# Optimization experiments

Hardware: AMD Instinct MI355X
Metric: run time of the kernel (lower is better)

Reference implementation:

```python
import jax, jax.numpy as jnp
import numpy as np

DIM = 768
HEADS = 12
HIDDEN = 3072
EPS = 1e-5


def _layernorm(x, g, b):
    mu = jnp.mean(x, axis=-1, keepdims=True)
    var = jnp.var(x, axis=-1, keepdims=True)
    return (x - mu) * jax.lax.rsqrt(var + EPS) * g + b


def setup_inputs() -> dict:
    key = jax.random.key(0)
    ks = jax.random.split(key, 10)
    s_in = 1.0 / np.sqrt(DIM)
    s_hid = 1.0 / np.sqrt(HIDDEN)
    return {
        "x": jax.random.normal(ks[0], (8, 1024, DIM), dtype=jnp.float32),
        "ln1_g": jnp.ones((DIM,), jnp.float32),
        "ln1_b": jnp.zeros((DIM,), jnp.float32),
        "qkv_w": jax.random.uniform(ks[1], (DIM, 3 * DIM), jnp.float32, -s_in, s_in),
        "qkv_b": jnp.zeros((3 * DIM,), jnp.float32),
        "proj_w": jax.random.uniform(ks[2], (DIM, DIM), jnp.float32, -s_in, s_in),
        "proj_b": jnp.zeros((DIM,), jnp.float32),
        "ln2_g": jnp.ones((DIM,), jnp.float32),
        "ln2_b": jnp.zeros((DIM,), jnp.float32),
        "fc1_w": jax.random.uniform(ks[3], (DIM, HIDDEN), jnp.float32, -s_in, s_in),
        "fc1_b": jnp.zeros((HIDDEN,), jnp.float32),
        "fc2_w": jax.random.uniform(ks[4], (HIDDEN, DIM), jnp.float32, -s_hid, s_hid),
        "fc2_b": jnp.zeros((DIM,), jnp.float32),
    }


def reference(x, ln1_g, ln1_b, qkv_w, qkv_b, proj_w, proj_b,
              ln2_g, ln2_b, fc1_w, fc1_b, fc2_w, fc2_b):
    B, N, C = x.shape
    H = HEADS
    Dh = C // H
    scale = Dh ** -0.5

    # --- attention sublayer (pre-norm) ---
    h = _layernorm(x, ln1_g, ln1_b)
    qkv = h @ qkv_w + qkv_b  # [B,N,3C]
    qkv = qkv.reshape(B, N, 3, H, Dh)
    q = qkv[:, :, 0].transpose(0, 2, 1, 3)  # [B,H,N,Dh]
    k = qkv[:, :, 1].transpose(0, 2, 1, 3)
    v = qkv[:, :, 2].transpose(0, 2, 1, 3)
    attn = jax.nn.softmax(jnp.einsum('bhnd,bhmd->bhnm', q, k) * scale, axis=-1)
    o = jnp.einsum('bhnm,bhmd->bhnd', attn, v)  # [B,H,N,Dh]
    o = o.transpose(0, 2, 1, 3).reshape(B, N, C)
    x = x + (o @ proj_w + proj_b)

    # --- MLP sublayer (pre-norm) ---
    h = _layernorm(x, ln2_g, ln2_b)
    h = jax.nn.gelu(h @ fc1_w + fc1_b, approximate=False)
    x = x + (h @ fc2_w + fc2_b)
    return x
```

## Files before the change

kernel.cpp:

```cpp
#include <hip/hip_runtime.h>
#include <math.h>

#define DIM    768
#define HEADS  12
#define HIDDEN 3072
#define SEQ    1024
#define NTOK   8192
#define QKVLD  2304

typedef __bf16 bf16_t;
typedef __bf16 bf16x4 __attribute__((ext_vector_type(4)));
typedef __bf16 bf16x8 __attribute__((ext_vector_type(8)));
typedef float  f32x4  __attribute__((ext_vector_type(4)));

union ABFrag { bf16x4 h[2]; bf16x8 v; };

__device__ __forceinline__ void gload16(const void* g, void* l) {
  __builtin_amdgcn_global_load_lds(
      (const __attribute__((address_space(1))) void*)g,
      (__attribute__((address_space(3))) void*)l, 16, 0, 0);
}

__device__ __forceinline__ f32x4 mfma16(bf16x8 a, bf16x8 b, f32x4 c) {
  return __builtin_amdgcn_mfma_f32_16x16x32_bf16(a, b, c, 0, 0, 0);
}

__device__ __forceinline__ ABFrag load_frag(const bf16_t* rowp, int g) {
  ABFrag f;
  f.h[0] = *(const bf16x4*)(rowp + 4 * g);
  f.h[1] = *(const bf16x4*)(rowp + 4 * g + 16);
  return f;
}

__device__ __forceinline__ ABFrag load_frag_swz(const bf16_t* base, int row, int e, int g) {
  const int o0 = e + 4 * g, o1 = o0 + 16;
  const int s = row & 7;
  const bf16_t* rp = base + row * 64;
  ABFrag f;
  f.h[0] = *(const bf16x4*)(rp + ((((o0 >> 3) ^ s) << 3) | (o0 & 7)));
  f.h[1] = *(const bf16x4*)(rp + ((((o1 >> 3) ^ s) << 3) | (o1 & 7)));
  return f;
}

__device__ __forceinline__ bf16x8 ldsfrag(const bf16_t* base, int row, int lc) {
  return *(const bf16x8*)(base + row * 64 + (((lc ^ (row & 7))) << 3));
}

__global__ __launch_bounds__(256) void ln_kernel(
    const float* __restrict__ x, const float* __restrict__ gw,
    const float* __restrict__ bw, bf16_t* __restrict__ out) {
  const int row = blockIdx.x;
  const int t = threadIdx.x;
  const float* xr = x + (size_t)row * DIM;
  float v0 = xr[t], v1 = xr[t + 256], v2 = xr[t + 512];
  float s = v0 + v1 + v2;
  float s2 = v0 * v0 + v1 * v1 + v2 * v2;
  #pragma unroll
  for (int o = 32; o > 0; o >>= 1) {
    s += __shfl_down(s, o);
    s2 += __shfl_down(s2, o);
  }
  __shared__ float red[8];
  if ((t & 63) == 0) { red[(t >> 6) * 2] = s; red[(t >> 6) * 2 + 1] = s2; }
  __syncthreads();
  float S  = red[0] + red[2] + red[4] + red[6];
  float S2 = red[1] + red[3] + red[5] + red[7];
  float mu  = S * (1.0f / DIM);
  float var = S2 * (1.0f / DIM) - mu * mu;
  float rs  = rsqrtf(var + 1e-5f);
  bf16_t* orow = out + (size_t)row * DIM;
  orow[t]       = (bf16_t)((v0 - mu) * rs * gw[t]       + bw[t]);
  orow[t + 256] = (bf16_t)((v1 - mu) * rs * gw[t + 256] + bw[t + 256]);
  orow[t + 512] = (bf16_t)((v2 - mu) * rs * gw[t + 512] + bw[t + 512]);
}

__global__ __launch_bounds__(256) void wtrans_kernel(
    const float* __restrict__ W, bf16_t* __restrict__ Wt, int K, int N) {
  __shared__ float tile[32][33];
  const int tx = threadIdx.x, ty = threadIdx.y;
  const int n0 = blockIdx.x * 32, k0 = blockIdx.y * 32;
  #pragma unroll
  for (int i = 0; i < 4; ++i)
    tile[ty + i * 8][tx] = W[(size_t)(k0 + ty + i * 8) * N + n0 + tx];
  __syncthreads();
  #pragma unroll
  for (int i = 0; i < 4; ++i)
    Wt[(size_t)(n0 + ty + i * 8) * K + k0 + tx] = (bf16_t)tile[tx][ty + i * 8];
}

__global__ __launch_bounds__(256) void vtrans_kernel(
    const bf16_t* __restrict__ qkv, bf16_t* __restrict__ vt) {
  __shared__ bf16_t tile[64][65];
  const int bh = blockIdx.y, b = bh / HEADS, h = bh % HEADS;
  const int n0 = blockIdx.x * 64;
  const int t = threadIdx.x;
  const int c = t & 63, rr = t >> 6;
  const bf16_t* src = qkv + (size_t)(b * SEQ + n0) * QKVLD + 2 * DIM + h * 64;
  #pragma unroll
  for (int i = 0; i < 16; ++i)
    tile[c][rr + i * 4] = src[(size_t)(rr + i * 4) * QKVLD + c];
  __syncthreads();
  bf16_t* dst = vt + (size_t)bh * 64 * SEQ + n0;
  #pragma unroll
  for (int i = 0; i < 16; ++i)
    dst[(size_t)(rr + i * 4) * SEQ + c] = tile[rr + i * 4][c];
}

template <int MODE, int BN>
__global__ __launch_bounds__(256) void gemm_bk64(
    const bf16_t* __restrict__ A, const bf16_t* __restrict__ Bt,
    int N, int K,
    const float* __restrict__ bias, const float* __restrict__ res,
    void* __restrict__ outv, int gx) {
  constexpr int WAVES_N = (BN == 128) ? 2 : 1;
  constexpr int WM = (BN == 128) ? 4 : 2;
  constexpr int WN = 4;
  __shared__ bf16_t sA[128 * 64];
  __shared__ bf16_t sB[BN * 64];
  const int tid = threadIdx.x;
  const int lane = tid & 63;
  const int wid = tid >> 6;
  const int g = lane >> 4, r16 = lane & 15;

  const int nwg = gridDim.x;
  const int cpx = nwg >> 3;
  const int sw = (blockIdx.x & 7) * cpx + (blockIdx.x >> 3);
  const int bx = sw % gx, by = sw / gx;
  const int row0 = by * 128, col0 = bx * BN;
  const int wr = (wid / WAVES_N) * (WM * 16);
  const int wc = (wid % WAVES_N) * (WN * 16);

  f32x4 acc[WM][WN];
  #pragma unroll
  for (int m = 0; m < WM; ++m)
    #pragma unroll
    for (int n = 0; n < WN; ++n) acc[m][n] = f32x4{0.f, 0.f, 0.f, 0.f};

  const int kSteps = K >> 6;
  for (int kt = 0; kt < kSteps; ++kt) {
    __syncthreads();
    #pragma unroll
    for (int rnd = 0; rnd < 4; ++rnd) {
      const int c = rnd * 256 + tid;
      const int row = c >> 3, scp = (c & 7) ^ (row & 7);
      gload16(A + (size_t)(row0 + row) * K + kt * 64 + scp * 8, &sA[c * 8]);
    }
    #pragma unroll
    for (int rnd = 0; rnd < BN / 32; ++rnd) {
      const int c = rnd * 256 + tid;
      const int row = c >> 3, scp = (c & 7) ^ (row & 7);
      gload16(Bt + (size_t)(col0 + row) * K + kt * 64 + scp * 8, &sB[c * 8]);
    }
    __syncthreads();
    bf16x8 af[WM][2], bfr[WN][2];
    #pragma unroll
    for (int m = 0; m < WM; ++m)
      #pragma unroll
      for (int kk = 0; kk < 2; ++kk)
        af[m][kk] = ldsfrag(sA, wr + m * 16 + r16, kk * 4 + g);
    #pragma unroll
    for (int n = 0; n < WN; ++n)
      #pragma unroll
      for (int kk = 0; kk < 2; ++kk)
        bfr[n][kk] = ldsfrag(sB, wc + n * 16 + r16, kk * 4 + g);
    #pragma unroll
    for (int kk = 0; kk < 2; ++kk)
      #pragma unroll
      for (int m = 0; m < WM; ++m)
        #pragma unroll
        for (int n = 0; n < WN; ++n)
          acc[m][n] = mfma16(af[m][kk], bfr[n][kk], acc[m][n]);
  }

  #pragma unroll
  for (int m = 0; m < WM; ++m) {
    const int rowb = row0 + wr + m * 16 + 4 * g;
    #pragma unroll
    for (int n = 0; n < WN; ++n) {
      const int col = col0 + wc + n * 16 + r16;
      const float bv = bias[col];
      #pragma unroll
      for (int r = 0; r < 4; ++r) {
        const size_t idx = (size_t)(rowb + r) * N + col;
        float v = acc[m][n][r] + bv;
        if (MODE == 0) {
          ((bf16_t*)outv)[idx] = (bf16_t)v;
        } else if (MODE == 1) {
          ((float*)outv)[idx] = v + res[idx];
        } else {
          float gv = 0.5f * v * (1.f + erff(v * 0.70710678118654752f));
          ((bf16_t*)outv)[idx] = (bf16_t)gv;
        }
      }
    }
  }
}

__global__ __launch_bounds__(256) void attn_kernel(
    const bf16_t* __restrict__ qkv, const bf16_t* __restrict__ vt,
    bf16_t* __restrict__ o) {
  __shared__ bf16_t kbuf[2][64 * 64];
  __shared__ bf16_t vbuf[2][64 * 64];
  const int bh = blockIdx.y, b = bh / HEADS, h = bh % HEADS;
  const int q0 = blockIdx.x * 64;
  const int tid = threadIdx.x, lane = tid & 63, wid = tid >> 6;
  const int g = lane >> 4, r16 = lane & 15;

  const bf16_t* qptr = qkv + (size_t)b * SEQ * QKVLD + h * 64;
  const bf16_t* kptr = qptr + DIM;
  const bf16_t* vtp  = vt + (size_t)bh * 64 * SEQ;

  ABFrag aq[2];
  {
    const bf16_t* qr = qptr + (size_t)(q0 + wid * 16 + r16) * QKVLD;
    aq[0] = load_frag(qr, g);
    aq[1] = load_frag(qr + 32, g);
  }

  float lacc = 0.f;
  f32x4 acco[4];
  #pragma unroll
  for (int n = 0; n < 4; ++n) acco[n] = f32x4{0.f, 0.f, 0.f, 0.f};

  auto stage = [&](int buf, int kv0) {
    #pragma unroll
    for (int rnd = 0; rnd < 2; ++rnd) {
      const int c = rnd * 256 + tid;
      const int row = c >> 3, scp = (c & 7) ^ (row & 7);
      gload16(kptr + (size_t)(kv0 + row) * QKVLD + scp * 8,
              &kbuf[buf][(rnd * 256 + wid * 64) * 8]);
    }
    #pragma unroll
    for (int rnd = 0; rnd < 2; ++rnd) {
      const int c = rnd * 256 + tid;
      const int row = c >> 3, scp = (c & 7) ^ (row & 7);
      gload16(vtp + (size_t)row * SEQ + kv0 + scp * 8,
              &vbuf[buf][(rnd * 256 + wid * 64) * 8]);
    }
  };

  const float C2 = 0.125f * 1.4426950408889634f;

  stage(0, 0);
  for (int it = 0; it < SEQ / 64; ++it) {
    const int cur = it & 1;
    __syncthreads();
    if (it + 1 < SEQ / 64) stage(cur ^ 1, (it + 1) * 64);

    f32x4 st[4];
    __builtin_amdgcn_s_setprio(1);
    #pragma unroll
    for (int t = 0; t < 4; ++t) {
      st[t] = f32x4{0.f, 0.f, 0.f, 0.f};
      ABFrag ak0 = load_frag_swz(kbuf[cur], t * 16 + r16, 0, g);
      st[t] = mfma16(ak0.v, aq[0].v, st[t]);
      ABFrag ak1 = load_frag_swz(kbuf[cur], t * 16 + r16, 32, g);
      st[t] = mfma16(ak1.v, aq[1].v, st[t]);
    }
    __builtin_amdgcn_s_setprio(0);

    float p[4][4];
    #pragma unroll
    for (int t = 0; t < 4; ++t)
      #pragma unroll
      for (int r = 0; r < 4; ++r) {
        float e = __builtin_amdgcn_exp2f(fmaf(st[t][r], C2, -16.0f));
        p[t][r] = e;
        lacc += e;
      }

    ABFrag pa0, pa1;
    #pragma unroll
    for (int r = 0; r < 4; ++r) {
      pa0.h[0][r] = (bf16_t)p[0][r];
      pa0.h[1][r] = (bf16_t)p[1][r];
      pa1.h[0][r] = (bf16_t)p[2][r];
      pa1.h[1][r] = (bf16_t)p[3][r];
    }

    __builtin_amdgcn_s_setprio(1);
    #pragma unroll
    for (int n = 0; n < 4; ++n) {
      ABFrag bv0 = load_frag_swz(vbuf[cur], n * 16 + r16, 0, g);
      acco[n] = mfma16(pa0.v, bv0.v, acco[n]);
      ABFrag bv1 = load_frag_swz(vbuf[cur], n * 16 + r16, 32, g);
      acco[n] = mfma16(pa1.v, bv1.v, acco[n]);
    }
    __builtin_amdgcn_s_setprio(0);
  }

  float lt = lacc;
  lt += __shfl_xor(lt, 16);
  lt += __shfl_xor(lt, 32);
  float linv[4];
  #pragma unroll
  for (int r = 0; r < 4; ++r) linv[r] = 1.0f / __shfl(lt, 4 * g + r);
  bf16_t* op = o + (size_t)(b * SEQ + q0 + wid * 16 + 4 * g) * DIM + h * 64;
  #pragma unroll
  for (int n = 0; n < 4; ++n)
    #pragma unroll
    for (int r = 0; r < 4; ++r)
      op[(size_t)r * DIM + n * 16 + r16] = (bf16_t)(acco[n][r] * linv[r]);
}

extern "C" void kernel_launch(void* const* d_in, const int* in_sizes, int n_in,
                              void* d_out, int out_size, void* d_ws, size_t ws_size,
                              hipStream_t stream) {
  const float* x      = (const float*)d_in[0];
  const float* ln1_g  = (const float*)d_in[1];
  const float* ln1_b  = (const float*)d_in[2];
  const float* qkv_w  = (const float*)d_in[3];
  const float* qkv_b  = (const float*)d_in[4];
  const float* proj_w = (const float*)d_in[5];
  const float* proj_b = (const float*)d_in[6];
  const float* ln2_g  = (const float*)d_in[7];
  const float* ln2_b  = (const float*)d_in[8];
  const float* fc1_w  = (const float*)d_in[9];
  const float* fc1_b  = (const float*)d_in[10];
  const float* fc2_w  = (const float*)d_in[11];
  const float* fc2_b  = (const float*)d_in[12];
  float* out = (float*)d_out;

  char* ws = (char*)d_ws;
  size_t off = 0;
  auto alloc = [&](size_t bytes) -> void* {
    void* p = ws + off;
    off += (bytes + 255) & ~(size_t)255;
    return p;
  };
  bf16_t* wqkvT  = (bf16_t*)alloc((size_t)QKVLD * DIM * 2);
  bf16_t* wprojT = (bf16_t*)alloc((size_t)DIM * DIM * 2);
  bf16_t* wfc1T  = (bf16_t*)alloc((size_t)HIDDEN * DIM * 2);
  bf16_t* wfc2T  = (bf16_t*)alloc((size_t)DIM * HIDDEN * 2);
  bf16_t* buf1   = (bf16_t*)alloc((size_t)NTOK * DIM * 2);
  bf16_t* buf2   = (bf16_t*)alloc((size_t)NTOK * HIDDEN * 2);
  bf16_t* buf3   = (bf16_t*)alloc((size_t)NTOK * DIM * 2);
  float*  x1     = (float*)alloc((size_t)NTOK * DIM * 4);

  bf16_t* h1 = buf1;     bf16_t* obf = buf1;
  bf16_t* qkvbf = buf2;  bf16_t* h3 = buf2;
  bf16_t* vt = buf3;     bf16_t* h2 = buf3;
  (void)in_sizes; (void)n_in; (void)out_size; (void)ws_size;

  dim3 tb(32, 8);
  wtrans_kernel<<<dim3(QKVLD / 32, DIM / 32), tb, 0, stream>>>(qkv_w, wqkvT, DIM, QKVLD);
  wtrans_kernel<<<dim3(DIM / 32, DIM / 32), tb, 0, stream>>>(proj_w, wprojT, DIM, DIM);
  wtrans_kernel<<<dim3(HIDDEN / 32, DIM / 32), tb, 0, stream>>>(fc1_w, wfc1T, DIM, HIDDEN);
  wtrans_kernel<<<dim3(DIM / 32, HIDDEN / 32), tb, 0, stream>>>(fc2_w, wfc2T, HIDDEN, DIM);

  ln_kernel<<<NTOK, 256, 0, stream>>>(x, ln1_g, ln1_b, h1);
  gemm_bk64<0, 128><<<(QKVLD / 128) * (NTOK / 128), 256, 0, stream>>>(
      h1, wqkvT, QKVLD, DIM, qkv_b, nullptr, qkvbf, QKVLD / 128);
  vtrans_kernel<<<dim3(SEQ / 64, 8 * HEADS), 256, 0, stream>>>(qkvbf, vt);
  attn_kernel<<<dim3(SEQ / 64, 8 * HEADS), 256, 0, stream>>>(qkvbf, vt, obf);
  gemm_bk64<1, 64><<<(DIM / 64) * (NTOK / 128), 256, 0, stream>>>(
      obf, wprojT, DIM, DIM, proj_b, x, x1, DIM / 64);
  ln_kernel<<<NTOK, 256, 0, stream>>>(x1, ln2_g, ln2_b, h2);
  gemm_bk64<2, 128><<<(HIDDEN / 128) * (NTOK / 128), 256, 0, stream>>>(
      h2, wfc1T, HIDDEN, DIM, fc1_b, nullptr, h3, HIDDEN / 128);
  gemm_bk64<1, 64><<<(DIM / 64) * (NTOK / 128), 256, 0, stream>>>(
      h3, wfc2T, DIM, HIDDEN, fc2_b, x1, out, DIM / 64);
}
```

Before: 269.0 us.

## Add 256x256 double-buffered 8-wave GEMM for QKV and FC1 projections

Adds a new 512-thread GEMM kernel with 256x256 output tiles, double-buffered LDS staging through global_load_lds, explicit vmcnt waits, setprio around the MFMA blocks, and an XCD-aware block swizzle. It replaces the 128-wide GEMM for the QKV and FC1 matmuls to raise operand reuse per LDS load and overlap loads with compute. The proj and FC2 GEMMs also move from BN=64 to BN=128 tiles. The large tiles use 128KB of LDS and many accumulator registers per thread, and they give fewer blocks (288 and 384), which may leave CUs idle or lower occupancy.

```diff
diff --git a/kernel.cpp b/kernel.cpp
--- a/kernel.cpp
+++ b/kernel.cpp
@@ -14,6 +14,10 @@
 typedef float  f32x4  __attribute__((ext_vector_type(4)));
 
 union ABFrag { bf16x4 h[2]; bf16x8 v; };
+
+#define VMCNT6() asm volatile("s_waitcnt vmcnt(6)" ::: "memory")
+#define VMCNT0() asm volatile("s_waitcnt vmcnt(0)" ::: "memory")
+#define LGKM0()  asm volatile("s_waitcnt lgkmcnt(0)" ::: "memory")
 
 __device__ __forceinline__ void gload16(const void* g, void* l) {
   __builtin_amdgcn_global_load_lds(
@@ -43,7 +47,7 @@
 }
 
 __device__ __forceinline__ bf16x8 ldsfrag(const bf16_t* base, int row, int lc) {
-  return *(const bf16x8*)(base + row * 64 + (((lc ^ (row & 7))) << 3));
+  return *(const bf16x8*)(base + row * 64 + ((lc ^ (row & 7)) << 3));
 }
 
 __global__ __launch_bounds__(256) void ln_kernel(
@@ -104,6 +108,124 @@
   #pragma unroll
   for (int i = 0; i < 16; ++i)
     dst[(size_t)(rr + i * 4) * SEQ + c] = tile[rr + i * 4][c];
+}
+
+template <int MODE>
+__global__ __launch_bounds__(512, 2) void gemm256(
+    const bf16_t* __restrict__ A, const bf16_t* __restrict__ Bt,
+    int N, int K, const float* __restrict__ bias,
+    bf16_t* __restrict__ outp, int gx) {
+  __shared__ bf16_t sA[2][256 * 64];
+  __shared__ bf16_t sB[2][256 * 64];
+  const int tid = threadIdx.x;
+  const int lane = tid & 63;
+  const int wid = tid >> 6;
+  const int g = lane >> 4, r16 = lane & 15;
+  const int wm = wid >> 2, wn = wid & 3;
+
+  const int nwg = gridDim.x;
+  const int cpx = nwg >> 3;
+  const int sw = (blockIdx.x & 7) * cpx + (blockIdx.x >> 3);
+  const int bx = sw % gx, by = sw / gx;
+  const int row0 = by * 256, col0 = bx * 256;
+
+  const int r0 = tid >> 3;
+  const int scp = (tid & 7) ^ (r0 & 7);
+  const bf16_t* aSrc = A + (size_t)(row0 + r0) * K + scp * 8;
+  const bf16_t* bSrc = Bt + (size_t)(col0 + r0) * K + scp * 8;
+
+  auto stageA = [&](int half, int kt, int p) {
+    const bf16_t* gsrc = aSrc + (size_t)(half * 128) * K + (size_t)kt * 64;
+    bf16_t* lb = &sA[p][half * 8192 + tid * 8];
+    gload16(gsrc, lb);
+    gload16(gsrc + (size_t)64 * K, lb + 4096);
+  };
+  auto stageB = [&](int half, int kt, int p) {
+    const bf16_t* gsrc = bSrc + (size_t)(half * 128) * K + (size_t)kt * 64;
+    bf16_t* lb = &sB[p][half * 8192 + tid * 8];
+    gload16(gsrc, lb);
+    gload16(gsrc + (size_t)64 * K, lb + 4096);
+  };
+
+  f32x4 acc[8][4];
+  #pragma unroll
+  for (int m = 0; m < 8; ++m)
+    #pragma unroll
+    for (int n = 0; n < 4; ++n) acc[m][n] = f32x4{0.f, 0.f, 0.f, 0.f};
+
+  const int nt = K >> 6;
+
+  stageB(0, 0, 0); stageB(1, 0, 0); stageA(0, 0, 0); stageA(1, 0, 0);
+  stageB(0, 1, 1); stageB(1, 1, 1); stageA(0, 1, 1);
+  VMCNT6();
+  __builtin_amdgcn_s_barrier();
+
+  for (int t = 0; t < nt; ++t) {
+    const int p = t & 1;
+    const bf16_t* pA = &sA[p][0];
+    const bf16_t* pB = &sB[p][0];
+    bf16x8 bfr[4][2];
+    #pragma unroll
+    for (int q = 0; q < 4; ++q) {
+      bf16x8 af[2][2];
+      #pragma unroll
+      for (int i = 0; i < 2; ++i)
+        #pragma unroll
+        for (int kk = 0; kk < 2; ++kk)
+          af[i][kk] = ldsfrag(pA, wm * 128 + (2 * q + i) * 16 + r16, kk * 4 + g);
+      if (q == 0) {
+        #pragma unroll
+        for (int n = 0; n < 4; ++n)
+          #pragma unroll
+          for (int kk = 0; kk < 2; ++kk)
+            bfr[n][kk] = ldsfrag(pB, wn * 64 + n * 16 + r16, kk * 4 + g);
+      }
+      if (q == 0) {
+        if (t + 1 < nt) stageA(1, t + 1, (t + 1) & 1);
+      } else if (q == 1) {
+        if (t + 2 < nt) stageB(0, t + 2, p);
+      } else if (q == 2) {
+        if (t + 2 < nt) stageB(1, t + 2, p);
+      } else {
+        if (t + 2 < nt) stageA(0, t + 2, p);
+        if (t + 1 < nt) { if (t + 2 < nt) VMCNT6(); else VMCNT0(); }
+      }
+      __builtin_amdgcn_s_barrier();
+      LGKM0();
+      __builtin_amdgcn_sched_barrier(0);
+      __builtin_amdgcn_s_setprio(1);
+      #pragma unroll
+      for (int kk = 0; kk < 2; ++kk)
+        #pragma unroll
+        for (int i = 0; i < 2; ++i)
+          #pragma unroll
+          for (int n = 0; n < 4; ++n)
+            acc[2 * q + i][n] = mfma16(af[i][kk], bfr[n][kk], acc[2 * q + i][n]);
+      __builtin_amdgcn_s_setprio(0);
+      __builtin_amdgcn_s_barrier();
+    }
+  }
+
+  #pragma unroll
+  for (int m = 0; m < 8; ++m) {
+    const int rowb = row0 + wm * 128 + m * 16 + 4 * g;
+    #pragma unroll
+    for (int n = 0; n < 4; ++n) {
+      const int col = col0 + wn * 64 + n * 16 + r16;
+      const float bv = bias[col];
+      #pragma unroll
+      for (int r = 0; r < 4; ++r) {
+        const size_t idx = (size_t)(rowb + r) * N + col;
+        float v = acc[m][n][r] + bv;
+        if (MODE == 0) {
+          outp[idx] = (bf16_t)v;
+        } else {
+          float gv = 0.5f * v * (1.f + erff(v * 0.70710678118654752f));
+          outp[idx] = (bf16_t)gv;
+        }
+      }
+    }
+  }
 }
 
 template <int MODE, int BN>
@@ -349,15 +471,15 @@
   wtrans_kernel<<<dim3(DIM / 32, HIDDEN / 32), tb, 0, stream>>>(fc2_w, wfc2T, HIDDEN, DIM);
 
   ln_kernel<<<NTOK, 256, 0, stream>>>(x, ln1_g, ln1_b, h1);
-  gemm_bk64<0, 128><<<(QKVLD / 128) * (NTOK / 128), 256, 0, stream>>>(
-      h1, wqkvT, QKVLD, DIM, qkv_b, nullptr, qkvbf, QKVLD / 128);
+  gemm256<0><<<(QKVLD / 256) * (NTOK / 256), 512, 0, stream>>>(
+      h1, wqkvT, QKVLD, DIM, qkv_b, qkvbf, QKVLD / 256);
   vtrans_kernel<<<dim3(SEQ / 64, 8 * HEADS), 256, 0, stream>>>(qkvbf, vt);
   attn_kernel<<<dim3(SEQ / 64, 8 * HEADS), 256, 0, stream>>>(qkvbf, vt, obf);
-  gemm_bk64<1, 64><<<(DIM / 64) * (NTOK / 128), 256, 0, stream>>>(
-      obf, wprojT, DIM, DIM, proj_b, x, x1, DIM / 64);
+  gemm_bk64<1, 128><<<(DIM / 128) * (NTOK / 128), 256, 0, stream>>>(
+      obf, wprojT, DIM, DIM, proj_b, x, x1, DIM / 128);
   ln_kernel<<<NTOK, 256, 0, stream>>>(x1, ln2_g, ln2_b, h2);
-  gemm_bk64<2, 128><<<(HIDDEN / 128) * (NTOK / 128), 256, 0, stream>>>(
-      h2, wfc1T, HIDDEN, DIM, fc1_b, nullptr, h3, HIDDEN / 128);
-  gemm_bk64<1, 64><<<(DIM / 64) * (NTOK / 128), 256, 0, stream>>>(
-      h3, wfc2T, DIM, HIDDEN, fc2_b, x1, out, DIM / 64);
-}
+  gemm256<2><<<(HIDDEN / 256) * (NTOK / 256), 512, 0, stream>>>(
+      h2, wfc1T, HIDDEN, DIM, fc1_b, h3, HIDDEN / 256);
+  gemm_bk64<1, 128><<<(DIM / 128) * (NTOK / 128), 256, 0, stream>>>(
+      h3, wfc2T, DIM, HIDDEN, fc2_b, x1, out, DIM / 128);
+}
```

New measurement: 312.1 us. 1.16x slower.

## Double-buffer GEMM LDS tiles and use 128x128 tiles for all GEMMs

Applied to the files above, without the earlier changes.

The GEMM kernel now keeps two LDS buffers for A and B and issues the global-to-LDS loads for the next K step before computing on the current one. This lets memory latency overlap with MFMA work and removes one barrier per iteration. The proj and fc2 GEMMs also move from 128x64 to 128x128 tiles, which halves their workgroup count (384 blocks) and doubles LDS per block to 64KB, so occupancy drops. There is also a risk: with a single barrier per iteration, the prefetch into the other buffer may race with waves that are still reading it from the previous step.

```diff
diff --git a/kernel.cpp b/kernel.cpp
--- a/kernel.cpp
+++ b/kernel.cpp
@@ -43,7 +43,7 @@
 }
 
 __device__ __forceinline__ bf16x8 ldsfrag(const bf16_t* base, int row, int lc) {
-  return *(const bf16x8*)(base + row * 64 + (((lc ^ (row & 7))) << 3));
+  return *(const bf16x8*)(base + row * 64 + ((lc ^ (row & 7)) << 3));
 }
 
 __global__ __launch_bounds__(256) void ln_kernel(
@@ -106,17 +106,14 @@
     dst[(size_t)(rr + i * 4) * SEQ + c] = tile[rr + i * 4][c];
 }
 
-template <int MODE, int BN>
-__global__ __launch_bounds__(256) void gemm_bk64(
+template <int MODE>
+__global__ __launch_bounds__(256) void gemm_db(
     const bf16_t* __restrict__ A, const bf16_t* __restrict__ Bt,
     int N, int K,
     const float* __restrict__ bias, const float* __restrict__ res,
     void* __restrict__ outv, int gx) {
-  constexpr int WAVES_N = (BN == 128) ? 2 : 1;
-  constexpr int WM = (BN == 128) ? 4 : 2;
-  constexpr int WN = 4;
-  __shared__ bf16_t sA[128 * 64];
-  __shared__ bf16_t sB[BN * 64];
+  __shared__ bf16_t sA[2][128 * 64];
+  __shared__ bf16_t sB[2][128 * 64];
   const int tid = threadIdx.x;
   const int lane = tid & 63;
   const int wid = tid >> 6;
@@ -126,57 +123,64 @@
   const int cpx = nwg >> 3;
   const int sw = (blockIdx.x & 7) * cpx + (blockIdx.x >> 3);
   const int bx = sw % gx, by = sw / gx;
-  const int row0 = by * 128, col0 = bx * BN;
-  const int wr = (wid / WAVES_N) * (WM * 16);
-  const int wc = (wid % WAVES_N) * (WN * 16);
-
-  f32x4 acc[WM][WN];
-  #pragma unroll
-  for (int m = 0; m < WM; ++m)
-    #pragma unroll
-    for (int n = 0; n < WN; ++n) acc[m][n] = f32x4{0.f, 0.f, 0.f, 0.f};
-
-  const int kSteps = K >> 6;
-  for (int kt = 0; kt < kSteps; ++kt) {
-    __syncthreads();
+  const int row0 = by * 128, col0 = bx * 128;
+  const int wr = (wid >> 1) * 64, wc = (wid & 1) * 64;
+
+  auto stage = [&](int p, int kt) {
     #pragma unroll
     for (int rnd = 0; rnd < 4; ++rnd) {
       const int c = rnd * 256 + tid;
       const int row = c >> 3, scp = (c & 7) ^ (row & 7);
-      gload16(A + (size_t)(row0 + row) * K + kt * 64 + scp * 8, &sA[c * 8]);
-    }
-    #pragma unroll
-    for (int rnd = 0; rnd < BN / 32; ++rnd) {
+      gload16(A + (size_t)(row0 + row) * K + (size_t)kt * 64 + scp * 8,
+              &sA[p][c * 8]);
+    }
+    #pragma unroll
+    for (int rnd = 0; rnd < 4; ++rnd) {
       const int c = rnd * 256 + tid;
       const int row = c >> 3, scp = (c & 7) ^ (row & 7);
-      gload16(Bt + (size_t)(col0 + row) * K + kt * 64 + scp * 8, &sB[c * 8]);
-    }
+      gload16(Bt + (size_t)(col0 + row) * K + (size_t)kt * 64 + scp * 8,
+              &sB[p][c * 8]);
+    }
+  };
+
+  f32x4 acc[4][4];
+  #pragma unroll
+  for (int m = 0; m < 4; ++m)
+    #pragma unroll
+    for (int n = 0; n < 4; ++n) acc[m][n] = f32x4{0.f, 0.f, 0.f, 0.f};
+
+  const int kSteps = K >> 6;
+  stage(0, 0);
+  for (int kt = 0; kt < kSteps; ++kt) {
+    const int cur = kt & 1;
     __syncthreads();
-    bf16x8 af[WM][2], bfr[WN][2];
-    #pragma unroll
-    for (int m = 0; m < WM; ++m)
+    if (kt + 1 < kSteps) stage(cur ^ 1, kt + 1);
+
+    bf16x8 af[4][2], bfr[4][2];
+    #pragma unroll
+    for (int m = 0; m < 4; ++m)
       #pragma unroll
       for (int kk = 0; kk < 2; ++kk)
-        af[m][kk] = ldsfrag(sA, wr + m * 16 + r16, kk * 4 + g);
-    #pragma unroll
-    for (int n = 0; n < WN; ++n)
+        af[m][kk] = ldsfrag(&sA[cur][0], wr + m * 16 + r16, kk * 4 + g);
+    #pragma unroll
+    for (int n = 0; n < 4; ++n)
       #pragma unroll
       for (int kk = 0; kk < 2; ++kk)
-        bfr[n][kk] = ldsfrag(sB, wc + n * 16 + r16, kk * 4 + g);
+        bfr[n][kk] = ldsfrag(&sB[cur][0], wc + n * 16 + r16, kk * 4 + g);
     #pragma unroll
     for (int kk = 0; kk < 2; ++kk)
       #pragma unroll
-      for (int m = 0; m < WM; ++m)
+      for (int m = 0; m < 4; ++m)
         #pragma unroll
-        for (int n = 0; n < WN; ++n)
+        for (int n = 0; n < 4; ++n)
           acc[m][n] = mfma16(af[m][kk], bfr[n][kk], acc[m][n]);
   }
 
   #pragma unroll
-  for (int m = 0; m < WM; ++m) {
+  for (int m = 0; m < 4; ++m) {
     const int rowb = row0 + wr + m * 16 + 4 * g;
     #pragma unroll
-    for (int n = 0; n < WN; ++n) {
+    for (int n = 0; n < 4; ++n) {
       const int col = col0 + wc + n * 16 + r16;
       const float bv = bias[col];
       #pragma unroll
@@ -349,15 +353,15 @@
   wtrans_kernel<<<dim3(DIM / 32, HIDDEN / 32), tb, 0, stream>>>(fc2_w, wfc2T, HIDDEN, DIM);
 
   ln_kernel<<<NTOK, 256, 0, stream>>>(x, ln1_g, ln1_b, h1);
-  gemm_bk64<0, 128><<<(QKVLD / 128) * (NTOK / 128), 256, 0, stream>>>(
+  gemm_db<0><<<(QKVLD / 128) * (NTOK / 128), 256, 0, stream>>>(
       h1, wqkvT, QKVLD, DIM, qkv_b, nullptr, qkvbf, QKVLD / 128);
   vtrans_kernel<<<dim3(SEQ / 64, 8 * HEADS), 256, 0, stream>>>(qkvbf, vt);
   attn_kernel<<<dim3(SEQ / 64, 8 * HEADS), 256, 0, stream>>>(qkvbf, vt, obf);
-  gemm_bk64<1, 64><<<(DIM / 64) * (NTOK / 128), 256, 0, stream>>>(
-      obf, wprojT, DIM, DIM, proj_b, x, x1, DIM / 64);
+  gemm_db<1><<<(DIM / 128) * (NTOK / 128), 256, 0, stream>>>(
+      obf, wprojT, DIM, DIM, proj_b, x, x1, DIM / 128);
   ln_kernel<<<NTOK, 256, 0, stream>>>(x1, ln2_g, ln2_b, h2);
-  gemm_bk64<2, 128><<<(HIDDEN / 128) * (NTOK / 128), 256, 0, stream>>>(
+  gemm_db<2><<<(HIDDEN / 128) * (NTOK / 128), 256, 0, stream>>>(
       h2, wfc1T, HIDDEN, DIM, fc1_b, nullptr, h3, HIDDEN / 128);
-  gemm_bk64<1, 64><<<(DIM / 64) * (NTOK / 128), 256, 0, stream>>>(
-      h3, wfc2T, DIM, HIDDEN, fc2_b, x1, out, DIM / 64);
-}
+  gemm_db<1><<<(DIM / 128) * (NTOK / 128), 256, 0, stream>>>(
+      h3, wfc2T, DIM, HIDDEN, fc2_b, x1, out, DIM / 128);
+}
```

Result: slower. 284.0 us (+5.6%).
